# Optimization experiments

Measured on AMD Instinct MI355X. Metric: run time of the kernel, lower is better.

The kernel has to match this reference:

```python
import jax, jax.numpy as jnp
import numpy as np
from jax import lax

BS, T, GRID, FEAT = 64, 32, 36, 256
HID, PROJ, NCLS = 256, 128, 6
MLP_IN = FEAT + HID  # 512


def _lstm(h, c, xs, Wih, Whh, bih, bhh):
    # xs: (L, bs, in); PyTorch gate order i, f, g, o
    def step(carry, x):
        h, c = carry
        g = x @ Wih.T + bih + h @ Whh.T + bhh
        i_, f_, g_, o_ = jnp.split(g, 4, axis=-1)
        c = jax.nn.sigmoid(f_) * c + jax.nn.sigmoid(i_) * jnp.tanh(g_)
        h = jax.nn.sigmoid(o_) * jnp.tanh(c)
        return (h, c), None
    (h, c), _ = lax.scan(step, (h, c), xs)
    return h, c


def setup_inputs() -> dict:
    key = jax.random.key(0)
    ks = iter(jax.random.split(key, 32))
    r = lambda *s: jax.random.normal(next(ks), s, dtype=jnp.float32) * 0.05
    inp = {
        'cnn_feat_seq': jax.random.normal(next(ks), (BS, T, GRID, FEAT), dtype=jnp.float32),
        'gaze_seq': jax.random.normal(next(ks), (BS, T, 3), dtype=jnp.float32),
        # spatial attention layer
        'W_lh': r(PROJ, HID), 'b_lh': r(PROJ),      # linear_lstm
        'W_cn': r(PROJ, FEAT), 'b_cn': r(PROJ),     # linear_cnn
        'w_wt': r(1, PROJ),                         # linear_weight (no bias)
        # gaze LSTM
        'Wih': r(4 * HID, 3), 'Whh': r(4 * HID, HID), 'bih': r(4 * HID), 'bhh': r(4 * HID),
        # init hidden / cell MLPs (Linear, Tanh, Linear, Tanh)
        'Wh1': r(HID, 3), 'bh1': r(HID), 'Wh2': r(HID, HID), 'bh2': r(HID),
        'Wc1': r(HID, 3), 'bc1': r(HID), 'Wc2': r(HID, HID), 'bc2': r(HID),
        # mlp classifier (3 linears, no activations)
        'Wm1': r(MLP_IN, MLP_IN), 'bm1': r(MLP_IN),
        'Wm2': r(MLP_IN, MLP_IN), 'bm2': r(MLP_IN),
        'Wm3': r(NCLS, MLP_IN), 'bm3': r(NCLS),
    }
    return inp


def reference(cnn_feat_seq, gaze_seq, W_lh, b_lh, W_cn, b_cn, w_wt,
              Wih, Whh, bih, bhh, Wh1, bh1, Wh2, bh2, Wc1, bc1, Wc2, bc2,
              Wm1, bm1, Wm2, bm2, Wm3, bm3):
    bs, num_frame, grid, feat = cnn_feat_seq.shape
    # init LSTM state: Sequential(Linear,Tanh,Linear,Tanh) then an extra F.tanh
    mg = jnp.mean(gaze_seq, axis=1)  # (bs, 3)
    h = jnp.tanh(jnp.tanh(jnp.tanh(mg @ Wh1.T + bh1) @ Wh2.T + bh2))
    c = jnp.tanh(jnp.tanh(jnp.tanh(mg @ Wc1.T + bc1) @ Wc2.T + bc2))

    preds = []
    for i in range(num_frame):
        V = cnn_feat_seq[:, i]  # (bs, grid, feat)
        # attention scores; same Linear applied per grid cell -> compute once
        Hl = h @ W_lh.T + b_lh                       # (bs, proj)
        Vp = V @ W_cn.T + b_cn                       # (bs, grid, proj)
        z = jnp.tanh(Hl[:, None, :] + Vp) @ w_wt[0]  # (bs, grid)
        # replicate torch.cat(dim=0).view(bs, grid): flat order is grid-major
        z_scrambled = z.T.reshape(bs, grid)
        sw = jax.nn.softmax(z_scrambled, axis=1)     # (bs, grid)
        spatial_feat = jnp.einsum('bgf,bg->bf', V, sw)
        # LSTM over growing gaze prefix (frame 0: first step only)
        L = 1 if i == 0 else i
        xs = jnp.transpose(gaze_seq[:, :L, :], (1, 0, 2))  # (L, bs, 3)
        h, c = _lstm(h, c, xs, Wih, Whh, bih, bhh)
        fc = jnp.concatenate([spatial_feat, h], axis=1)    # (bs, 512)
        pred = ((fc @ Wm1.T + bm1) @ Wm2.T + bm2) @ Wm3.T + bm3
        preds.append(pred[None])  # (1, bs, ncls)
    # torch.cat(pred_all, 1) over (1,bs,ncls) pieces -> (1, T*bs, ncls)
    return jnp.concatenate(preds, axis=1)
```

## Files before the change

### kernel.cpp

```cpp
#include <hip/hip_runtime.h>
#include <math.h>


typedef _Float16 h2_t __attribute__((ext_vector_type(2)));

#if __has_builtin(__builtin_amdgcn_fdot2)
#define HAVE_FDOT2 1
#else
#define HAVE_FDOT2 0
#endif

__device__ __forceinline__ float dot2(unsigned w, unsigned h, float acc) {
#if HAVE_FDOT2
  return __builtin_amdgcn_fdot2(__builtin_bit_cast(h2_t, w),
                                __builtin_bit_cast(h2_t, h), acc, false);
#else
  h2_t a = __builtin_bit_cast(h2_t, w);
  h2_t b = __builtin_bit_cast(h2_t, h);
  return acc + (float)a[0] * (float)b[0] + (float)a[1] * (float)b[1];
#endif
}

__device__ __forceinline__ unsigned pack2(float a, float b) {
  h2_t p;
  p[0] = (_Float16)a;
  p[1] = (_Float16)b;
  return __builtin_bit_cast(unsigned, p);
}

__device__ __forceinline__ float sigmoid_f(float x) {
  return __builtin_amdgcn_rcpf(1.f + __expf(-x));
}
__device__ __forceinline__ float tanh_f(float x) {
  return 1.f - 2.f * __builtin_amdgcn_rcpf(1.f + __expf(2.f * x));
}

__global__ void k_pack_wv(const float* __restrict__ Whh,
                          unsigned* __restrict__ wv_pack,
                          unsigned* __restrict__ wlds_pack) {
  const int idx = blockIdx.x * 256 + threadIdx.x;
  if (idx < 98304) {
    const int m = idx >> 10, tau = idx & 1023;
    const int pair = 32 + m;
    wv_pack[idx] = pack2(Whh[tau * 256 + 2 * pair], Whh[tau * 256 + 2 * pair + 1]);
  } else {
    const int j = idx - 98304;
    const int row = j >> 5, pair = j & 31;
    wlds_pack[j] = pack2(Whh[row * 256 + 2 * pair], Whh[row * 256 + 2 * pair + 1]);
  }
}

__global__ void k_packh2(const float* __restrict__ src,
                         unsigned* __restrict__ dst, int n) {
  const int i = blockIdx.x * 256 + threadIdx.x;
  if (i < n) dst[i] = pack2(src[2 * i], src[2 * i + 1]);
}

__global__ void k_xg(const float* __restrict__ gaze,
                     const float* __restrict__ Wih,
                     const float* __restrict__ bih,
                     const float* __restrict__ bhh,
                     float* __restrict__ xg) {
  const int idx = blockIdx.x * 256 + threadIdx.x;
  if (idx >= 31 * 64 * 1024) return;
  const int j = idx & 1023;
  const int b = (idx >> 10) & 63;
  const int t = idx >> 16;
  const float* gz = gaze + (b * 32 + t) * 3;
  xg[idx] = gz[0] * Wih[j * 3 + 0] + gz[1] * Wih[j * 3 + 1] +
            gz[2] * Wih[j * 3 + 2] + bih[j] + bhh[j];
}

__global__ void k_init(const float* __restrict__ gaze,
                       const float* __restrict__ Wh1, const float* __restrict__ bh1,
                       const float* __restrict__ Wh2, const float* __restrict__ bh2,
                       const float* __restrict__ Wc1, const float* __restrict__ bc1,
                       const float* __restrict__ Wc2, const float* __restrict__ bc2,
                       float* __restrict__ HH, float* __restrict__ c0) {
  const int b = blockIdx.x;
  const int tid = threadIdx.x;
  __shared__ float mg[3];
  __shared__ float t1h[256], t1c[256];
  if (tid < 3) {
    float s = 0.f;
    for (int t = 0; t < 32; t++) s += gaze[(b * 32 + t) * 3 + tid];
    mg[tid] = s * (1.f / 32.f);
  }
  __syncthreads();
  {
    float a = mg[0] * Wh1[tid * 3 + 0] + mg[1] * Wh1[tid * 3 + 1] +
              mg[2] * Wh1[tid * 3 + 2] + bh1[tid];
    t1h[tid] = tanhf(a);
    float c = mg[0] * Wc1[tid * 3 + 0] + mg[1] * Wc1[tid * 3 + 1] +
              mg[2] * Wc1[tid * 3 + 2] + bc1[tid];
    t1c[tid] = tanhf(c);
  }
  __syncthreads();
  float s1 = bh2[tid], s2 = bc2[tid];
  for (int k = 0; k < 256; k++) {
    s1 += t1h[k] * Wh2[tid * 256 + k];
    s2 += t1c[k] * Wc2[tid * 256 + k];
  }
  HH[b * 256 + tid] = tanhf(tanhf(s1));
  c0[b * 256 + tid] = tanhf(tanhf(s2));
}

__global__ __launch_bounds__(1024) void k_lstm(
    const float* __restrict__ xg, const unsigned* __restrict__ wv_pack,
    const unsigned* __restrict__ wlds_pack, const float* __restrict__ c0,
    float* __restrict__ HH) {
  const int b = blockIdx.x;
  const int tid = threadIdx.x;
  __shared__ __align__(16) unsigned wlds[1024 * 36];
  __shared__ float actl[1024];
  __shared__ __align__(16) unsigned h2l[128];

  for (int i = tid; i < 1024 * 32; i += 1024) {
    const int row = i >> 5, p = i & 31;
    wlds[row * 36 + p] = wlds_pack[i];
  }
  unsigned wv[96];
  {
    const unsigned* wvp = wv_pack + tid;
#define LD1(m) wv[(m)] = wvp[(m) * 1024];
#define LD8(m) LD1(m) LD1((m) + 1) LD1((m) + 2) LD1((m) + 3) \
               LD1((m) + 4) LD1((m) + 5) LD1((m) + 6) LD1((m) + 7)
    LD8(0) LD8(8) LD8(16) LD8(24) LD8(32) LD8(40)
    LD8(48) LD8(56) LD8(64) LD8(72) LD8(80) LD8(88)
#undef LD1
#undef LD8
  }

  float cst = (tid < 256) ? c0[b * 256 + tid] : 0.f;
  if (tid < 256) ((_Float16*)h2l)[tid] = (_Float16)HH[b * 256 + tid];
  __syncthreads();

  const unsigned* wA = &wlds[tid * 36];
  const bool is_g = (tid >= 512) & (tid < 768);
  float hval = 0.f;

  for (int frame = 0; frame < 32; frame++) {
    const int L = frame ? frame : 1;
    for (int t = 0; t < L; t++) {
      const float xgv = xg[(t * 64 + b) * 1024 + tid];
      float ga0 = 0.f, ga1 = 0.f;
#pragma unroll
      for (int q = 0; q < 8; q++) {
        const uint4 h4 = *(const uint4*)&h2l[4 * q];
        const uint4 a4 = *(const uint4*)&wA[4 * q];
        if ((q & 1) == 0) {
          ga0 = dot2(a4.x, h4.x, ga0);
          ga0 = dot2(a4.y, h4.y, ga0);
          ga0 = dot2(a4.z, h4.z, ga0);
          ga0 = dot2(a4.w, h4.w, ga0);
        } else {
          ga1 = dot2(a4.x, h4.x, ga1);
          ga1 = dot2(a4.y, h4.y, ga1);
          ga1 = dot2(a4.z, h4.z, ga1);
          ga1 = dot2(a4.w, h4.w, ga1);
        }
      }
#pragma unroll
      for (int q = 0; q < 24; q++) {
        const uint4 h4 = *(const uint4*)&h2l[32 + 4 * q];
        if ((q & 1) == 0) {
          ga0 = dot2(wv[4 * q + 0], h4.x, ga0);
          ga0 = dot2(wv[4 * q + 1], h4.y, ga0);
          ga0 = dot2(wv[4 * q + 2], h4.z, ga0);
          ga0 = dot2(wv[4 * q + 3], h4.w, ga0);
        } else {
          ga1 = dot2(wv[4 * q + 0], h4.x, ga1);
          ga1 = dot2(wv[4 * q + 1], h4.y, ga1);
          ga1 = dot2(wv[4 * q + 2], h4.z, ga1);
          ga1 = dot2(wv[4 * q + 3], h4.w, ga1);
        }
      }
      const float g = ga0 + ga1 + xgv;
      const float act = is_g ? tanh_f(g) : sigmoid_f(g);
      actl[tid] = act;
      __syncthreads();
      if (tid < 256) {
        const float i_ = actl[tid];
        const float f_ = actl[256 + tid];
        const float g_ = actl[512 + tid];
        const float o_ = actl[768 + tid];
        cst = f_ * cst + i_ * g_;
        hval = o_ * tanh_f(cst);
        ((_Float16*)h2l)[tid] = (_Float16)hval;
      }
      __syncthreads();
    }
    if (tid < 256) HH[((frame + 1) * 64 + b) * 256 + tid] = hval;
  }
}

__global__ void k_hl(const float* __restrict__ HH,
                     const unsigned* __restrict__ wlh_h2,
                     const float* __restrict__ blh, float* __restrict__ Hl) {
  const int i = blockIdx.x;
  const int tid = threadIdx.x;
  __shared__ __align__(16) unsigned Ah[64 * 132];
  __shared__ __align__(16) unsigned Bh[128 * 132];
  for (int idx = tid; idx < 64 * 128; idx += 256) {
    const int r = idx >> 7, kp = idx & 127;
    const float* s = HH + ((size_t)(i * 64 + r)) * 256 + 2 * kp;
    Ah[r * 132 + kp] = pack2(s[0], s[1]);
  }
  for (int idx = tid; idx < 128 * 128; idx += 256) {
    const int o = idx >> 7, kp = idx & 127;
    Bh[o * 132 + kp] = wlh_h2[o * 128 + kp];
  }
  __syncthreads();
  const int ry = tid >> 4, px = tid & 15;
  float acc[4][8];
#pragma unroll
  for (int k = 0; k < 4; k++)
#pragma unroll
    for (int j = 0; j < 8; j++) acc[k][j] = 0.f;
  for (int kb = 0; kb < 32; kb++) {
    uint4 a4[4], b4[8];
#pragma unroll
    for (int k = 0; k < 4; k++) a4[k] = *(const uint4*)&Ah[(16 * k + ry) * 132 + 4 * kb];
#pragma unroll
    for (int j = 0; j < 8; j++) b4[j] = *(const uint4*)&Bh[(16 * j + px) * 132 + 4 * kb];
#pragma unroll
    for (int k = 0; k < 4; k++)
#pragma unroll
      for (int j = 0; j < 8; j++) {
        acc[k][j] = dot2(a4[k].x, b4[j].x, acc[k][j]);
        acc[k][j] = dot2(a4[k].y, b4[j].y, acc[k][j]);
        acc[k][j] = dot2(a4[k].z, b4[j].z, acc[k][j]);
        acc[k][j] = dot2(a4[k].w, b4[j].w, acc[k][j]);
      }
  }
#pragma unroll
  for (int k = 0; k < 4; k++)
#pragma unroll
    for (int j = 0; j < 8; j++)
      Hl[(i * 64 + 16 * k + ry) * 128 + 16 * j + px] = acc[k][j] + blh[16 * j + px];
}

__global__ void k_att_z(const float* __restrict__ cnn,
                        const unsigned* __restrict__ wcn_h2,
                        const float* __restrict__ bcn,
                        const float* __restrict__ Hl,
                        const float* __restrict__ wwt,
                        float* __restrict__ zbuf) {
  const int bid = blockIdx.x;
  const int i = bid / 18, rt = bid - 18 * i;
  const int tid = threadIdx.x;
  const int r0 = rt * 128;
  __shared__ __align__(16) unsigned As[128 * 132];
  __shared__ __align__(16) unsigned Bs[128 * 132];
  __shared__ float zpart[128 * 16];
  __shared__ float Hls[5 * 128];
  __shared__ float wws[128];
  __shared__ float bcs[128];

  for (int idx = tid; idx < 128 * 128; idx += 256) {
    const int r = idx >> 7, kp = idx & 127;
    const int R = r0 + r;
    const int b = R / 36, g = R - b * 36;
    const float* src = cnn + (((size_t)b * 32 + i) * 36 + g) * 256 + 2 * kp;
    As[r * 132 + kp] = pack2(src[0], src[1]);
  }
  for (int idx = tid; idx < 128 * 128; idx += 256) {
    const int o = idx >> 7, kp = idx & 127;
    Bs[o * 132 + kp] = wcn_h2[o * 128 + kp];
  }
  const int bmin = r0 / 36;
  for (int idx = tid; idx < 5 * 128; idx += 256) {
    const int bb = bmin + (idx >> 7);
    if (bb < 64) Hls[idx] = Hl[(i * 64 + bb) * 128 + (idx & 127)];
  }
  if (tid < 128) {
    wws[tid] = wwt[tid];
    bcs[tid] = bcn[tid];
  }
  __syncthreads();

  const int ry = tid >> 4, px = tid & 15;
  float acc[8][8];
#pragma unroll
  for (int k = 0; k < 8; k++)
#pragma unroll
    for (int j = 0; j < 8; j++) acc[k][j] = bcs[16 * j + px];
  for (int kb = 0; kb < 32; kb++) {
    uint4 a4[8], b4[8];
#pragma unroll
    for (int k = 0; k < 8; k++) a4[k] = *(const uint4*)&As[(16 * k + ry) * 132 + 4 * kb];
#pragma unroll
    for (int j = 0; j < 8; j++) b4[j] = *(const uint4*)&Bs[(16 * j + px) * 132 + 4 * kb];
#pragma unroll
    for (int k = 0; k < 8; k++)
#pragma unroll
      for (int j = 0; j < 8; j++) {
        acc[k][j] = dot2(a4[k].x, b4[j].x, acc[k][j]);
        acc[k][j] = dot2(a4[k].y, b4[j].y, acc[k][j]);
        acc[k][j] = dot2(a4[k].z, b4[j].z, acc[k][j]);
        acc[k][j] = dot2(a4[k].w, b4[j].w, acc[k][j]);
      }
  }
#pragma unroll
  for (int k = 0; k < 8; k++) {
    const int r = 16 * k + ry;
    const int R = r0 + r;
    const int b = R / 36;
    const float* HlRow = &Hls[(b - bmin) * 128];
    float zp = 0.f;
#pragma unroll
    for (int j = 0; j < 8; j++) {
      const int po = 16 * j + px;
      zp += wws[po] * tanh_f(HlRow[po] + acc[k][j]);
    }
    zpart[r * 16 + px] = zp;
  }
  __syncthreads();
  if (tid < 128) {
    float z = 0.f;
#pragma unroll
    for (int x = 0; x < 16; x++) z += zpart[tid * 16 + x];
    const int R = r0 + tid;
    const int b = R / 36, g = R - b * 36;
    zbuf[(i * 64 + b) * 36 + g] = z;
  }
}

__global__ void k_att_sf(const float* __restrict__ cnn,
                         const float* __restrict__ zbuf,
                         const float* __restrict__ HH,
                         float* __restrict__ fc) {
  const int bid = blockIdx.x;
  const int i = bid >> 6, b = bid & 63;
  const int tid = threadIdx.x;
  __shared__ float zl[36];
  __shared__ float el[40];
  __shared__ float red[1];
  if (tid < 36) {
    const int idx = b * 36 + tid;
    zl[tid] = zbuf[(i * 64 + (idx & 63)) * 36 + (idx >> 6)];
  }
  __syncthreads();
  if (tid == 0) {
    float m = zl[0];
    for (int g = 1; g < 36; g++) m = fmaxf(m, zl[g]);
    float s = 0.f;
    for (int g = 0; g < 36; g++) {
      const float e = __expf(zl[g] - m);
      el[g] = e;
      s += e;
    }
    red[0] = 1.f / s;
  }
  __syncthreads();
  const float inv = red[0];
  float accv = 0.f;
  const float* Vb = cnn + (((size_t)b * 32 + i) * 36) * 256 + tid;
#pragma unroll 4
  for (int g = 0; g < 36; g++) accv += el[g] * Vb[g * 256];
  fc[(size_t)bid * 512 + tid] = accv * inv;
  fc[(size_t)bid * 512 + 256 + tid] = HH[((i + 1) * 64 + b) * 256 + tid];
}

template <int SRCMODE>
__global__ void k_mlp(const void* __restrict__ src,
                      const unsigned* __restrict__ wh2,
                      const float* __restrict__ bias,
                      unsigned* __restrict__ dst) {
  const int bid = blockIdx.x;
  const int nb = bid >> 2, ob = bid & 3;
  const int n0 = nb * 64, o0 = ob * 128;
  const int tid = threadIdx.x;
  __shared__ __align__(16) unsigned As[64 * 132];
  __shared__ __align__(16) unsigned Bs[128 * 132];
  const int ry = tid >> 4, px = tid & 15;
  float acc[4][8];
#pragma unroll
  for (int k = 0; k < 4; k++)
#pragma unroll
    for (int m = 0; m < 8; m++)
      acc[k][m] = bias[o0 + 32 * (m >> 1) + 2 * px + (m & 1)];
  for (int kc = 0; kc < 2; kc++) {
    __syncthreads();
    for (int idx = tid; idx < 64 * 128; idx += 256) {
      const int r = idx >> 7, kp = idx & 127;
      if (SRCMODE == 0) {
        const float* s = (const float*)src + ((size_t)(n0 + r)) * 512 + kc * 256 + 2 * kp;
        As[r * 132 + kp] = pack2(s[0], s[1]);
      } else {
        As[r * 132 + kp] = ((const unsigned*)src)[((size_t)(n0 + r)) * 256 + kc * 128 + kp];
      }
    }
    for (int idx = tid; idx < 128 * 128; idx += 256) {
      const int o = idx >> 7, kp = idx & 127;
      Bs[o * 132 + kp] = wh2[((size_t)(o0 + o)) * 256 + kc * 128 + kp];
    }
    __syncthreads();
    for (int kb = 0; kb < 32; kb++) {
      uint4 a4[4], b4[8];
#pragma unroll
      for (int k = 0; k < 4; k++)
        a4[k] = *(const uint4*)&As[(16 * k + ry) * 132 + 4 * kb];
#pragma unroll
      for (int m = 0; m < 8; m++)
        b4[m] = *(const uint4*)&Bs[(32 * (m >> 1) + 2 * px + (m & 1)) * 132 + 4 * kb];
#pragma unroll
      for (int k = 0; k < 4; k++)
#pragma unroll
        for (int m = 0; m < 8; m++) {
          acc[k][m] = dot2(a4[k].x, b4[m].x, acc[k][m]);
          acc[k][m] = dot2(a4[k].y, b4[m].y, acc[k][m]);
          acc[k][m] = dot2(a4[k].z, b4[m].z, acc[k][m]);
          acc[k][m] = dot2(a4[k].w, b4[m].w, acc[k][m]);
        }
    }
  }
#pragma unroll
  for (int k = 0; k < 4; k++) {
    const int n = n0 + 16 * k + ry;
#pragma unroll
    for (int j = 0; j < 4; j++)
      dst[(size_t)n * 256 + (o0 >> 1) + 16 * j + px] =
          pack2(acc[k][2 * j], acc[k][2 * j + 1]);
  }
}

__global__ void k_mlp3(const unsigned* __restrict__ y2h2,
                       const unsigned* __restrict__ wm3h2,
                       const float* __restrict__ bm3,
                       float* __restrict__ out) {
  const int nb = blockIdx.x;
  const int tid = threadIdx.x;
  __shared__ __align__(16) unsigned Ys[64 * 256];
  __shared__ __align__(16) unsigned Ws[6 * 256];
  for (int idx = tid; idx < 64 * 256; idx += 256)
    Ys[idx] = y2h2[(size_t)nb * 64 * 256 + idx];
  for (int idx = tid; idx < 6 * 256; idx += 256) Ws[idx] = wm3h2[idx];
  __syncthreads();
  for (int u = 0; u < 2; u++) {
    const int idx = tid + u * 256;
    if (idx < 384) {
      const int nl = idx / 6, c = idx - 6 * nl;
      float a0 = 0.f, a1 = 0.f;
#pragma unroll
      for (int kq = 0; kq < 64; kq++) {
        const uint4 y4 = *(const uint4*)&Ys[nl * 256 + 4 * kq];
        const uint4 w4 = *(const uint4*)&Ws[c * 256 + 4 * kq];
        a0 = dot2(y4.x, w4.x, a0);
        a1 = dot2(y4.y, w4.y, a1);
        a0 = dot2(y4.z, w4.z, a0);
        a1 = dot2(y4.w, w4.w, a1);
      }
      out[(size_t)(nb * 64 + nl) * 6 + c] = a0 + a1 + bm3[c];
    }
  }
}

extern "C" void kernel_launch(void* const* d_in, const int* in_sizes, int n_in,
                              void* d_out, int out_size, void* d_ws,
                              size_t ws_size, hipStream_t stream) {
  (void)in_sizes; (void)n_in; (void)out_size; (void)ws_size;
  const float* cnn  = (const float*)d_in[0];
  const float* gaze = (const float*)d_in[1];
  const float* W_lh = (const float*)d_in[2];
  const float* b_lh = (const float*)d_in[3];
  const float* W_cn = (const float*)d_in[4];
  const float* b_cn = (const float*)d_in[5];
  const float* w_wt = (const float*)d_in[6];
  const float* Wih  = (const float*)d_in[7];
  const float* Whh  = (const float*)d_in[8];
  const float* bih  = (const float*)d_in[9];
  const float* bhh  = (const float*)d_in[10];
  const float* Wh1  = (const float*)d_in[11];
  const float* bh1  = (const float*)d_in[12];
  const float* Wh2  = (const float*)d_in[13];
  const float* bh2  = (const float*)d_in[14];
  const float* Wc1  = (const float*)d_in[15];
  const float* bc1  = (const float*)d_in[16];
  const float* Wc2  = (const float*)d_in[17];
  const float* bc2  = (const float*)d_in[18];
  const float* Wm1  = (const float*)d_in[19];
  const float* bm1  = (const float*)d_in[20];
  const float* Wm2  = (const float*)d_in[21];
  const float* bm2  = (const float*)d_in[22];
  const float* Wm3  = (const float*)d_in[23];
  const float* bm3  = (const float*)d_in[24];
  float* out = (float*)d_out;

  unsigned* W = (unsigned*)d_ws;
  float* Wf = (float*)d_ws;
  const size_t O_xg  = 0;
  const size_t O_wv  = 2031616;
  const size_t O_wl  = O_wv + 98304;
  const size_t O_HH  = O_wl + 32768;
  const size_t O_c0  = O_HH + 540672;
  const size_t O_Hl  = O_c0 + 16384;
  const size_t O_z   = O_Hl + 262144;
  const size_t O_fc  = O_z + 73728;
  const size_t O_y1  = O_fc + 1048576;
  const size_t O_y2  = O_y1 + 524288;
  const size_t O_wcn = O_y2 + 524288;
  const size_t O_wlh = O_wcn + 16384;
  const size_t O_wm1 = O_wlh + 16384;
  const size_t O_wm2 = O_wm1 + 131072;
  const size_t O_wm3 = O_wm2 + 131072;

  float* xg  = Wf + O_xg;
  float* HH  = Wf + O_HH;
  float* c0f = Wf + O_c0;
  float* Hlf = Wf + O_Hl;
  float* zf  = Wf + O_z;
  float* fcf = Wf + O_fc;

  k_pack_wv<<<512, 256, 0, stream>>>(Whh, W + O_wv, W + O_wl);
  k_packh2<<<64, 256, 0, stream>>>(W_cn, W + O_wcn, 16384);
  k_packh2<<<64, 256, 0, stream>>>(W_lh, W + O_wlh, 16384);
  k_packh2<<<512, 256, 0, stream>>>(Wm1, W + O_wm1, 131072);
  k_packh2<<<512, 256, 0, stream>>>(Wm2, W + O_wm2, 131072);
  k_packh2<<<6, 256, 0, stream>>>(Wm3, W + O_wm3, 1536);
  k_xg<<<7936, 256, 0, stream>>>(gaze, Wih, bih, bhh, xg);
  k_init<<<64, 256, 0, stream>>>(gaze, Wh1, bh1, Wh2, bh2, Wc1, bc1, Wc2, bc2,
                                 HH, c0f);
  k_lstm<<<64, 1024, 0, stream>>>(xg, W + O_wv, W + O_wl, c0f, HH);
  k_hl<<<32, 256, 0, stream>>>(HH, W + O_wlh, b_lh, Hlf);
  k_att_z<<<576, 256, 0, stream>>>(cnn, W + O_wcn, b_cn, Hlf, w_wt, zf);
  k_att_sf<<<2048, 256, 0, stream>>>(cnn, zf, HH, fcf);
  k_mlp<0><<<128, 256, 0, stream>>>((const void*)fcf, W + O_wm1, bm1, W + O_y1);
  k_mlp<1><<<128, 256, 0, stream>>>((const void*)(W + O_y1), W + O_wm2, bm2, W + O_y2);
  k_mlp3<<<32, 256, 0, stream>>>(W + O_y2, W + O_wm3, bm3, out);
}
```

Baseline: 1.199 ms.

## Overlap LSTM recurrence with h-independent attention projection and weight packing

The sequential LSTM kernel, which occupies only 64 blocks, is fused into one launch with extra blocks. These blocks compute the h-independent V@W_cn projection into an fp16 buffer and pack the MLP and W_lh weights, so that work runs concurrently on idle CUs. A new k_zfin kernel then finishes the attention scores from the precomputed projection, and falls back to the old kernel when the workspace is too small. The LSTM's register-cached weights (96 registers per thread) are replaced by uint4 global/L2 loads each step, which lowers register pressure but adds memory latency on the serial critical path.

```diff
diff --git a/kernel.cpp b/kernel.cpp
--- a/kernel.cpp
+++ b/kernel.cpp
@@ -35,18 +35,19 @@
   return 1.f - 2.f * __builtin_amdgcn_rcpf(1.f + __expf(2.f * x));
 }
 
-__global__ void k_pack_wv(const float* __restrict__ Whh,
-                          unsigned* __restrict__ wv_pack,
-                          unsigned* __restrict__ wlds_pack) {
+__global__ void k_pack_lstm(const float* __restrict__ Whh,
+                            unsigned* __restrict__ wlds_pack,
+                            unsigned* __restrict__ wst) {
   const int idx = blockIdx.x * 256 + threadIdx.x;
-  if (idx < 98304) {
-    const int m = idx >> 10, tau = idx & 1023;
-    const int pair = 32 + m;
-    wv_pack[idx] = pack2(Whh[tau * 256 + 2 * pair], Whh[tau * 256 + 2 * pair + 1]);
+  if (idx < 32768) {
+    const int row = idx >> 5, pair = idx & 31;
+    wlds_pack[idx] =
+        pack2(Whh[row * 256 + 2 * pair], Whh[row * 256 + 2 * pair + 1]);
   } else {
-    const int j = idx - 98304;
-    const int row = j >> 5, pair = j & 31;
-    wlds_pack[j] = pack2(Whh[row * 256 + 2 * pair], Whh[row * 256 + 2 * pair + 1]);
+    const int rel = idx - 32768;
+    const int m = rel >> 12, row = (rel >> 2) & 1023, d = rel & 3;
+    const int pair = 32 + 4 * m + d;
+    wst[rel] = pack2(Whh[row * 256 + 2 * pair], Whh[row * 256 + 2 * pair + 1]);
   }
 }
 
@@ -105,92 +106,212 @@
   c0[b * 256 + tid] = tanhf(tanhf(s2));
 }
 
-__global__ __launch_bounds__(1024) void k_lstm(
-    const float* __restrict__ xg, const unsigned* __restrict__ wv_pack,
+__global__ __launch_bounds__(1024) void k_fused(
+    const float* __restrict__ xg, const unsigned* __restrict__ wst,
     const unsigned* __restrict__ wlds_pack, const float* __restrict__ c0,
-    float* __restrict__ HH) {
-  const int b = blockIdx.x;
-  const int tid = threadIdx.x;
-  __shared__ __align__(16) unsigned wlds[1024 * 36];
-  __shared__ float actl[1024];
-  __shared__ __align__(16) unsigned h2l[128];
-
-  for (int i = tid; i < 1024 * 32; i += 1024) {
-    const int row = i >> 5, p = i & 31;
-    wlds[row * 36 + p] = wlds_pack[i];
-  }
-  unsigned wv[96];
-  {
-    const unsigned* wvp = wv_pack + tid;
-#define LD1(m) wv[(m)] = wvp[(m) * 1024];
-#define LD8(m) LD1(m) LD1((m) + 1) LD1((m) + 2) LD1((m) + 3) \
-               LD1((m) + 4) LD1((m) + 5) LD1((m) + 6) LD1((m) + 7)
-    LD8(0) LD8(8) LD8(16) LD8(24) LD8(32) LD8(40)
-    LD8(48) LD8(56) LD8(64) LD8(72) LD8(80) LD8(88)
-#undef LD1
-#undef LD8
-  }
-
-  float cst = (tid < 256) ? c0[b * 256 + tid] : 0.f;
-  if (tid < 256) ((_Float16*)h2l)[tid] = (_Float16)HH[b * 256 + tid];
-  __syncthreads();
-
-  const unsigned* wA = &wlds[tid * 36];
-  const bool is_g = (tid >= 512) & (tid < 768);
-  float hval = 0.f;
-
-  for (int frame = 0; frame < 32; frame++) {
-    const int L = frame ? frame : 1;
-    for (int t = 0; t < L; t++) {
-      const float xgv = xg[(t * 64 + b) * 1024 + tid];
-      float ga0 = 0.f, ga1 = 0.f;
-#pragma unroll
-      for (int q = 0; q < 8; q++) {
-        const uint4 h4 = *(const uint4*)&h2l[4 * q];
-        const uint4 a4 = *(const uint4*)&wA[4 * q];
-        if ((q & 1) == 0) {
-          ga0 = dot2(a4.x, h4.x, ga0);
-          ga0 = dot2(a4.y, h4.y, ga0);
-          ga0 = dot2(a4.z, h4.z, ga0);
-          ga0 = dot2(a4.w, h4.w, ga0);
-        } else {
-          ga1 = dot2(a4.x, h4.x, ga1);
-          ga1 = dot2(a4.y, h4.y, ga1);
-          ga1 = dot2(a4.z, h4.z, ga1);
-          ga1 = dot2(a4.w, h4.w, ga1);
+    float* __restrict__ HH, const float* __restrict__ cnn,
+    const unsigned* __restrict__ wcn_h2, const float* __restrict__ bcn,
+    unsigned* __restrict__ Vp, int nvp, const float* __restrict__ Wm1,
+    unsigned* __restrict__ wm1d, const float* __restrict__ Wm2,
+    unsigned* __restrict__ wm2d, const float* __restrict__ Wm3,
+    unsigned* __restrict__ wm3d, const float* __restrict__ Wlh,
+    unsigned* __restrict__ wlhd) {
+  const int bid = blockIdx.x;
+  const int tid = threadIdx.x;
+  __shared__ __align__(16) unsigned smem[38016];
+
+  if (bid < 64) {
+    const int b = bid;
+    unsigned* wlds = smem;
+    float* actl = (float*)(smem + 36864);
+    unsigned* h2l = smem + 36864 + 1024;
+
+    for (int i = tid; i < 1024 * 32; i += 1024) {
+      const int row = i >> 5, p = i & 31;
+      wlds[row * 36 + p] = wlds_pack[i];
+    }
+
+    float cst = (tid < 256) ? c0[b * 256 + tid] : 0.f;
+    if (tid < 256) ((_Float16*)h2l)[tid] = (_Float16)HH[b * 256 + tid];
+    __syncthreads();
+
+    const unsigned* wA = &wlds[tid * 36];
+    const uint4* wstp = (const uint4*)wst + tid;
+    const bool is_g = (tid >= 512) & (tid < 768);
+    float hval = 0.f;
+
+    for (int frame = 0; frame < 32; frame++) {
+      const int L = frame ? frame : 1;
+      for (int t = 0; t < L; t++) {
+        const float xgv = xg[(t * 64 + b) * 1024 + tid];
+        float ga0 = 0.f, ga1 = 0.f;
+#pragma unroll
+        for (int q = 0; q < 8; q++) {
+          const uint4 h4 = *(const uint4*)&h2l[4 * q];
+          const uint4 a4 = *(const uint4*)&wA[4 * q];
+          if ((q & 1) == 0) {
+            ga0 = dot2(a4.x, h4.x, ga0);
+            ga0 = dot2(a4.y, h4.y, ga0);
+            ga0 = dot2(a4.z, h4.z, ga0);
+            ga0 = dot2(a4.w, h4.w, ga0);
+          } else {
+            ga1 = dot2(a4.x, h4.x, ga1);
+            ga1 = dot2(a4.y, h4.y, ga1);
+            ga1 = dot2(a4.z, h4.z, ga1);
+            ga1 = dot2(a4.w, h4.w, ga1);
+          }
         }
+#pragma unroll
+        for (int m = 0; m < 24; m++) {
+          const uint4 wq = wstp[m << 10];
+          const uint4 h4 = *(const uint4*)&h2l[32 + 4 * m];
+          if ((m & 1) == 0) {
+            ga0 = dot2(wq.x, h4.x, ga0);
+            ga0 = dot2(wq.y, h4.y, ga0);
+            ga0 = dot2(wq.z, h4.z, ga0);
+            ga0 = dot2(wq.w, h4.w, ga0);
+          } else {
+            ga1 = dot2(wq.x, h4.x, ga1);
+            ga1 = dot2(wq.y, h4.y, ga1);
+            ga1 = dot2(wq.z, h4.z, ga1);
+            ga1 = dot2(wq.w, h4.w, ga1);
+          }
+        }
+        const float g = ga0 + ga1 + xgv;
+        const float act = is_g ? tanh_f(g) : sigmoid_f(g);
+        actl[tid] = act;
+        __syncthreads();
+        if (tid < 256) {
+          const float i_ = actl[tid];
+          const float f_ = actl[256 + tid];
+          const float g_ = actl[512 + tid];
+          const float o_ = actl[768 + tid];
+          cst = f_ * cst + i_ * g_;
+          hval = o_ * tanh_f(cst);
+          ((_Float16*)h2l)[tid] = (_Float16)hval;
+        }
+        __syncthreads();
       }
-#pragma unroll
-      for (int q = 0; q < 24; q++) {
-        const uint4 h4 = *(const uint4*)&h2l[32 + 4 * q];
-        if ((q & 1) == 0) {
-          ga0 = dot2(wv[4 * q + 0], h4.x, ga0);
-          ga0 = dot2(wv[4 * q + 1], h4.y, ga0);
-          ga0 = dot2(wv[4 * q + 2], h4.z, ga0);
-          ga0 = dot2(wv[4 * q + 3], h4.w, ga0);
-        } else {
-          ga1 = dot2(wv[4 * q + 0], h4.x, ga1);
-          ga1 = dot2(wv[4 * q + 1], h4.y, ga1);
-          ga1 = dot2(wv[4 * q + 2], h4.z, ga1);
-          ga1 = dot2(wv[4 * q + 3], h4.w, ga1);
+      if (tid < 256) HH[((frame + 1) * 64 + b) * 256 + tid] = hval;
+    }
+  } else if (bid < 64 + nvp) {
+    const int vb = bid - 64;
+    const int i = vb / 18, rt = vb - 18 * i;
+    const int r0 = rt * 128;
+    unsigned* As = smem;
+    unsigned* Bs = smem + 16896;
+    float* bcs = (float*)(smem + 33792);
+
+    for (int idx = tid; idx < 128 * 128; idx += 1024) {
+      const int r = idx >> 7, kp = idx & 127;
+      const int R = r0 + r;
+      const int b = R / 36, g = R - b * 36;
+      const float* src = cnn + (((size_t)b * 32 + i) * 36 + g) * 256 + 2 * kp;
+      As[r * 132 + kp] = pack2(src[0], src[1]);
+    }
+    for (int idx = tid; idx < 128 * 128; idx += 1024) {
+      const int o = idx >> 7, kp = idx & 127;
+      Bs[o * 132 + kp] = wcn_h2[o * 128 + kp];
+    }
+    if (tid < 128) bcs[tid] = bcn[tid];
+    __syncthreads();
+
+    const int ry = tid >> 4, px = tid & 15;
+    float acc[2][8];
+#pragma unroll
+    for (int k = 0; k < 2; k++)
+#pragma unroll
+      for (int m = 0; m < 8; m++)
+        acc[k][m] = bcs[32 * (m >> 1) + 2 * px + (m & 1)];
+    for (int kb = 0; kb < 32; kb++) {
+      uint4 a4[2], b4[8];
+#pragma unroll
+      for (int k = 0; k < 2; k++)
+        a4[k] = *(const uint4*)&As[(64 * k + ry) * 132 + 4 * kb];
+#pragma unroll
+      for (int m = 0; m < 8; m++)
+        b4[m] = *(const uint4*)&Bs[(32 * (m >> 1) + 2 * px + (m & 1)) * 132 + 4 * kb];
+#pragma unroll
+      for (int k = 0; k < 2; k++)
+#pragma unroll
+        for (int m = 0; m < 8; m++) {
+          acc[k][m] = dot2(a4[k].x, b4[m].x, acc[k][m]);
+          acc[k][m] = dot2(a4[k].y, b4[m].y, acc[k][m]);
+          acc[k][m] = dot2(a4[k].z, b4[m].z, acc[k][m]);
+          acc[k][m] = dot2(a4[k].w, b4[m].w, acc[k][m]);
         }
-      }
-      const float g = ga0 + ga1 + xgv;
-      const float act = is_g ? tanh_f(g) : sigmoid_f(g);
-      actl[tid] = act;
-      __syncthreads();
-      if (tid < 256) {
-        const float i_ = actl[tid];
-        const float f_ = actl[256 + tid];
-        const float g_ = actl[512 + tid];
-        const float o_ = actl[768 + tid];
-        cst = f_ * cst + i_ * g_;
-        hval = o_ * tanh_f(cst);
-        ((_Float16*)h2l)[tid] = (_Float16)hval;
-      }
-      __syncthreads();
-    }
-    if (tid < 256) HH[((frame + 1) * 64 + b) * 256 + tid] = hval;
+    }
+#pragma unroll
+    for (int k = 0; k < 2; k++) {
+      const int R = r0 + 64 * k + ry;
+#pragma unroll
+      for (int jj = 0; jj < 4; jj++)
+        Vp[((size_t)i * 2304 + R) * 64 + 16 * jj + px] =
+            pack2(acc[k][2 * jj], acc[k][2 * jj + 1]);
+    }
+  } else {
+    const int pb = bid - 64 - nvp;
+    if (pb < 8) {
+      const int base = pb * 16384;
+      for (int j = tid; j < 16384; j += 1024)
+        wm1d[base + j] = pack2(Wm1[2 * (base + j)], Wm1[2 * (base + j) + 1]);
+    } else if (pb < 16) {
+      const int base = (pb - 8) * 16384;
+      for (int j = tid; j < 16384; j += 1024)
+        wm2d[base + j] = pack2(Wm2[2 * (base + j)], Wm2[2 * (base + j) + 1]);
+    } else {
+      for (int j = tid; j < 1536; j += 1024)
+        wm3d[j] = pack2(Wm3[2 * j], Wm3[2 * j + 1]);
+      for (int j = tid; j < 16384; j += 1024)
+        wlhd[j] = pack2(Wlh[2 * j], Wlh[2 * j + 1]);
+    }
+  }
+}
+
+__global__ void k_zfin(const unsigned* __restrict__ Vp,
+                       const float* __restrict__ Hl,
+                       const float* __restrict__ wwt,
+                       float* __restrict__ zbuf) {
+  const int bid = blockIdx.x;
+  const int i = bid / 18, rt = bid - 18 * i;
+  const int r0 = rt * 128;
+  const int tid = threadIdx.x;
+  __shared__ float Hls[5 * 128];
+  __shared__ float wws[128];
+  __shared__ float zpart[128 * 16];
+  const int bmin = r0 / 36;
+  for (int idx = tid; idx < 5 * 128; idx += 256) {
+    const int bb = bmin + (idx >> 7);
+    if (bb < 64) Hls[idx] = Hl[(i * 64 + bb) * 128 + (idx & 127)];
+  }
+  if (tid < 128) wws[tid] = wwt[tid];
+  __syncthreads();
+  const int ry = tid >> 4, px = tid & 15;
+#pragma unroll
+  for (int k = 0; k < 8; k++) {
+    const int r = 16 * k + ry;
+    const int R = r0 + r;
+    const int b = R / 36;
+    const unsigned* vr = Vp + ((size_t)i * 2304 + R) * 64;
+    const float* Hr = &Hls[(b - bmin) * 128];
+    float z = 0.f;
+#pragma unroll
+    for (int jj = 0; jj < 4; jj++) {
+      const int pp = 16 * jj + px;
+      const h2_t pr = __builtin_bit_cast(h2_t, vr[pp]);
+      z += wws[2 * pp] * tanh_f(Hr[2 * pp] + (float)pr[0]);
+      z += wws[2 * pp + 1] * tanh_f(Hr[2 * pp + 1] + (float)pr[1]);
+    }
+    zpart[r * 16 + px] = z;
+  }
+  __syncthreads();
+  if (tid < 128) {
+    float z = 0.f;
+#pragma unroll
+    for (int x = 0; x < 16; x++) z += zpart[tid * 16 + x];
+    const int R = r0 + tid;
+    const int b = R / 36, g = R - b * 36;
+    zbuf[(i * 64 + b) * 36 + g] = z;
   }
 }
 
@@ -459,7 +580,7 @@
 extern "C" void kernel_launch(void* const* d_in, const int* in_sizes, int n_in,
                               void* d_out, int out_size, void* d_ws,
                               size_t ws_size, hipStream_t stream) {
-  (void)in_sizes; (void)n_in; (void)out_size; (void)ws_size;
+  (void)in_sizes; (void)n_in; (void)out_size;
   const float* cnn  = (const float*)d_in[0];
   const float* gaze = (const float*)d_in[1];
   const float* W_lh = (const float*)d_in[2];
@@ -490,9 +611,9 @@
   unsigned* W = (unsigned*)d_ws;
   float* Wf = (float*)d_ws;
   const size_t O_xg  = 0;
-  const size_t O_wv  = 2031616;
-  const size_t O_wl  = O_wv + 98304;
-  const size_t O_HH  = O_wl + 32768;
+  const size_t O_wl  = 2031616;
+  const size_t O_wst = O_wl + 32768;
+  const size_t O_HH  = O_wst + 98304;
   const size_t O_c0  = O_HH + 540672;
   const size_t O_Hl  = O_c0 + 16384;
   const size_t O_z   = O_Hl + 262144;
@@ -504,6 +625,11 @@
   const size_t O_wm1 = O_wlh + 16384;
   const size_t O_wm2 = O_wm1 + 131072;
   const size_t O_wm3 = O_wm2 + 131072;
+  const size_t O_vp  = O_wm3 + 1536;
+  const size_t needed = (O_vp + 4718592) * 4ull;
+
+  const bool big = ws_size >= needed;
+  const int nvp = big ? 576 : 0;
 
   float* xg  = Wf + O_xg;
   float* HH  = Wf + O_HH;
@@ -511,19 +637,21 @@
   float* Hlf = Wf + O_Hl;
   float* zf  = Wf + O_z;
   float* fcf = Wf + O_fc;
-
-  k_pack_wv<<<512, 256, 0, stream>>>(Whh, W + O_wv, W + O_wl);
+  unsigned* Vp = W + O_vp;
+
+  k_pack_lstm<<<512, 256, 0, stream>>>(Whh, W + O_wl, W + O_wst);
   k_packh2<<<64, 256, 0, stream>>>(W_cn, W + O_wcn, 16384);
-  k_packh2<<<64, 256, 0, stream>>>(W_lh, W + O_wlh, 16384);
-  k_packh2<<<512, 256, 0, stream>>>(Wm1, W + O_wm1, 131072);
-  k_packh2<<<512, 256, 0, stream>>>(Wm2, W + O_wm2, 131072);
-  k_packh2<<<6, 256, 0, stream>>>(Wm3, W + O_wm3, 1536);
   k_xg<<<7936, 256, 0, stream>>>(gaze, Wih, bih, bhh, xg);
   k_init<<<64, 256, 0, stream>>>(gaze, Wh1, bh1, Wh2, bh2, Wc1, bc1, Wc2, bc2,
                                  HH, c0f);
-  k_lstm<<<64, 1024, 0, stream>>>(xg, W + O_wv, W + O_wl, c0f, HH);
+  k_fused<<<64 + nvp + 17, 1024, 0, stream>>>(
+      xg, W + O_wst, W + O_wl, c0f, HH, cnn, W + O_wcn, b_cn, Vp, nvp, Wm1,
+      W + O_wm1, Wm2, W + O_wm2, Wm3, W + O_wm3, W_lh, W + O_wlh);
   k_hl<<<32, 256, 0, stream>>>(HH, W + O_wlh, b_lh, Hlf);
-  k_att_z<<<576, 256, 0, stream>>>(cnn, W + O_wcn, b_cn, Hlf, w_wt, zf);
+  if (big)
+    k_zfin<<<576, 256, 0, stream>>>(Vp, Hlf, w_wt, zf);
+  else
+    k_att_z<<<576, 256, 0, stream>>>(cnn, W + O_wcn, b_cn, Hlf, w_wt, zf);
   k_att_sf<<<2048, 256, 0, stream>>>(cnn, zf, HH, fcf);
   k_mlp<0><<<128, 256, 0, stream>>>((const void*)fcf, W + O_wm1, bm1, W + O_y1);
   k_mlp<1><<<128, 256, 0, stream>>>((const void*)(W + O_y1), W + O_wm2, bm2, W + O_y2);
```

New measurement: 1.073 ms (median of 3 runs). 1.12x faster.
